# Performance work log

Measured on AMD Instinct MI355X. Metric: run time of the kernel, lower is better.

Reference implementation:

```python
import jax, jax.numpy as jnp
import numpy as np

B, T, I, H, O = 64, 512, 128, 1024, 128
FORGET_BIAS = 1.0  # TF LSTMCell default


def setup_inputs() -> dict:
    key = jax.random.key(0)
    k1, k2, k3 = jax.random.split(key, 3)
    X = jax.random.normal(k1, (B, T, I), dtype=jnp.float32)
    Wk = jax.random.normal(k2, (I + H, 4 * H), dtype=jnp.float32) * 0.02
    b = jnp.zeros((4 * H,), dtype=jnp.float32)
    Wd = jax.random.normal(k3, (H, O), dtype=jnp.float32) * 0.02
    bd = jnp.zeros((O,), dtype=jnp.float32)
    return {"X": X, "Wk": Wk, "b": b, "Wd": Wd, "bd": bd}


def _lstm(X, Wk, b):
    # TF LSTMCell with activation=relu; gate order in kernel: i, j, f, o
    batch = X.shape[0]
    h = X.shape[-1]  # not used; keep shapes explicit below
    c0 = jnp.zeros((batch, H), dtype=X.dtype)
    h0 = jnp.zeros((batch, H), dtype=X.dtype)

    def step(carry, x_t):
        c, hs = carry
        z = jnp.concatenate([x_t, hs], axis=-1) @ Wk + b  # [B, 4H]
        i, j, f, o = jnp.split(z, 4, axis=-1)
        i = jax.nn.sigmoid(i)
        f = jax.nn.sigmoid(f + FORGET_BIAS)
        o = jax.nn.sigmoid(o)
        g = jax.nn.relu(j)          # cell-input activation (custom relu)
        c_new = f * c + i * g
        h_new = o * jax.nn.relu(c_new)  # output activation (custom relu)
        return (c_new, h_new), h_new

    xs = jnp.swapaxes(X, 0, 1)  # [T, B, I]
    _, hs = jax.lax.scan(step, (c0, h0), xs)
    return jnp.swapaxes(hs, 0, 1)  # [B, T, H]


def reference(X, Wk, b, Wd, bd):
    rnn_out = _lstm(X, Wk, b)          # [B, T, H]
    outputs = rnn_out @ Wd + bd        # [B, T, O] (SL=True: dense per timestep)
    return outputs
```

## Files before the change

### kernel.cpp

```cpp
#include <hip/hip_runtime.h>
#include <math.h>

#define Bsz 64
#define Tn  512
#define In  128
#define Hn  1024
#define KT  1152
#define NBLK 128

#define GARR0 0
#define GFLG0 512

typedef __attribute__((ext_vector_type(8))) short bf16x8;
typedef __attribute__((ext_vector_type(4))) short s16x4;
typedef __attribute__((ext_vector_type(4))) float f32x4;
typedef __attribute__((ext_vector_type(4))) int   i32x4;

__device__ void llvm_amdgcn_raw_buffer_store_i16(short vdata, i32x4 srsrc, int voffset, int soffset, int cpol) __asm("llvm.amdgcn.raw.buffer.store.i16");

__device__ __forceinline__ i32x4 make_srd(const void* p, int bytes) {
  i32x4 r;
  r.x = (int)(unsigned)(unsigned long long)p;
  r.y = (int)((unsigned long long)p >> 32);
  r.z = bytes;
  r.w = 0x00020000;
  return r;
}

__device__ __forceinline__ unsigned short f2bf(float f) {
  union { float f; unsigned u; } x; x.f = f;
  unsigned r = x.u + 0x7FFFu + ((x.u >> 16) & 1u);
  return (unsigned short)(r >> 16);
}
__device__ __forceinline__ float sigmoidf_(float x) { return 1.0f / (1.0f + __expf(-x)); }

__global__ __launch_bounds__(256) void cast_x_kernel(const float* __restrict__ in,
                                                     unsigned short* __restrict__ out) {
  int i = blockIdx.x * 256 + threadIdx.x;
  f32x4 v = ((const f32x4*)in)[i];
  s16x4 o;
  o.x = (short)f2bf(v.x); o.y = (short)f2bf(v.y);
  o.z = (short)f2bf(v.z); o.w = (short)f2bf(v.w);
  ((s16x4*)out)[i] = o;
}

__global__ __launch_bounds__(256) void transpose_cast_kernel(const float* __restrict__ in,
                                                             unsigned short* __restrict__ out,
                                                             int R, int C, int ldo, int tilesR) {
  __shared__ unsigned short tile[64][73];
  int br = blockIdx.x % tilesR, bc = blockIdx.x / tilesR;
  int r0 = br << 6, c0 = bc << 6;
  for (int e = threadIdx.x; e < 4096; e += 256) {
    int r = e >> 6, c = e & 63;
    tile[r][c] = f2bf(in[(size_t)(r0 + r) * C + (c0 + c)]);
  }
  __syncthreads();
  for (int e = threadIdx.x; e < 4096; e += 256) {
    int c = e >> 6, r = e & 63;
    out[(size_t)(c0 + c) * ldo + (r0 + r)] = tile[r][c];
  }
}

__global__ __launch_bounds__(512, 1) void lstm_kernel(
    const unsigned short* __restrict__ Xb,
    const unsigned short* __restrict__ WkT,
    const float* __restrict__ bias,
    unsigned short* __restrict__ hs,
    unsigned* __restrict__ S)
{
  __shared__ float Z4[4][64][36];
  const int tid = threadIdx.x;
  const int blk = blockIdx.x;
  const int grp = blk >> 4;
  const int w   = tid >> 6;
  const int mh  = w & 1;
  const int kq  = w >> 1;
  const int l   = tid & 63, q = l >> 4, n16 = l & 15;

  const i32x4 hsrd = make_srd(hs, Tn * Bsz * Hn * 2);

  bf16x8 Bf[2][9];
#pragma unroll
  for (int nt = 0; nt < 2; ++nt) {
    int cl   = nt * 16 + n16;
    int gcol = (cl >> 3) * Hn + blk * 8 + (cl & 7);
    const unsigned short* bp = WkT + (size_t)gcol * KT + kq * 288 + q * 8;
#pragma unroll
    for (int ks = 0; ks < 9; ++ks)
      Bf[nt][ks] = *(const bf16x8*)(bp + ks * 32);
  }

  const int eb = tid >> 3, ej = tid & 7;
  const float bi  = bias[           blk * 8 + ej];
  const float bg  = bias[    Hn   + blk * 8 + ej];
  const float bfg = bias[2 * Hn   + blk * 8 + ej] + 1.0f;
  const float bo  = bias[3 * Hn   + blk * 8 + ej];
  const int   hst_off = (eb * Hn + blk * 8 + ej) * 2;
  float cst = 0.0f;

  const int b0 = mh * 32 + n16;
  const int b1 = b0 + 16;

  const unsigned needm = (kq == 0) ? 0x03u : (kq == 1) ? 0x0Eu : (kq == 2) ? 0x38u : 0xE0u;
  const bool mine = (l < 8) && ((needm >> l) & 1u);

  for (int t = 0; t < Tn; ++t) {
    f32x4 a00 = {0,0,0,0}, a01 = {0,0,0,0}, a10 = {0,0,0,0}, a11 = {0,0,0,0};

    if (t > 0) {
      bf16x8 X0[4], X1[4];
      if (kq == 0) {
#pragma unroll
        for (int ks = 0; ks < 4; ++ks) {
          X0[ks] = *(const bf16x8*)(Xb + ((size_t)b0 * Tn + t) * In + ks * 32 + q * 8);
          X1[ks] = *(const bf16x8*)(Xb + ((size_t)b1 * Tn + t) * In + ks * 32 + q * 8);
        }
      }
      for (;;) {
        unsigned f = mine ? __hip_atomic_load(&S[GFLG0 + 32 * l], __ATOMIC_RELAXED,
                                              __HIP_MEMORY_SCOPE_AGENT)
                          : 0xFFFFFFFFu;
        if (__ballot(f >= (unsigned)t) == ~0ull) break;
        __builtin_amdgcn_s_sleep(1);
      }
      const unsigned short* hrow = hs + (size_t)(t - 1) * (Bsz * Hn);
#pragma unroll
      for (int ks = 0; ks < 9; ++ks) {
        bf16x8 A0, A1;
        if (kq == 0 && ks < 4) {
          A0 = X0[ks]; A1 = X1[ks];
        } else {
          int kh = kq * 288 + ks * 32 - 128 + q * 8;
          A0 = *(const bf16x8*)(hrow + (size_t)b0 * Hn + kh);
          A1 = *(const bf16x8*)(hrow + (size_t)b1 * Hn + kh);
        }
        a00 = __builtin_amdgcn_mfma_f32_16x16x32_bf16(A0, Bf[0][ks], a00, 0, 0, 0);
        a01 = __builtin_amdgcn_mfma_f32_16x16x32_bf16(A0, Bf[1][ks], a01, 0, 0, 0);
        a10 = __builtin_amdgcn_mfma_f32_16x16x32_bf16(A1, Bf[0][ks], a10, 0, 0, 0);
        a11 = __builtin_amdgcn_mfma_f32_16x16x32_bf16(A1, Bf[1][ks], a11, 0, 0, 0);
      }
    } else if (kq == 0) {
#pragma unroll
      for (int ks = 0; ks < 4; ++ks) {
        bf16x8 A0 = *(const bf16x8*)(Xb + ((size_t)b0 * Tn) * In + ks * 32 + q * 8);
        bf16x8 A1 = *(const bf16x8*)(Xb + ((size_t)b1 * Tn) * In + ks * 32 + q * 8);
        a00 = __builtin_amdgcn_mfma_f32_16x16x32_bf16(A0, Bf[0][ks], a00, 0, 0, 0);
        a01 = __builtin_amdgcn_mfma_f32_16x16x32_bf16(A0, Bf[1][ks], a01, 0, 0, 0);
        a10 = __builtin_amdgcn_mfma_f32_16x16x32_bf16(A1, Bf[0][ks], a10, 0, 0, 0);
        a11 = __builtin_amdgcn_mfma_f32_16x16x32_bf16(A1, Bf[1][ks], a11, 0, 0, 0);
      }
    }

#pragma unroll
    for (int r = 0; r < 4; ++r) {
      int row = mh * 32 + q * 4 + r;
      Z4[kq][row     ][     n16] = a00[r];
      Z4[kq][row     ][16 + n16] = a01[r];
      Z4[kq][row + 16][     n16] = a10[r];
      Z4[kq][row + 16][16 + n16] = a11[r];
    }
    __syncthreads();

    float zi = bi, zg = bg, zf = bfg, zo = bo;
#pragma unroll
    for (int k2 = 0; k2 < 4; ++k2) {
      zi += Z4[k2][eb][     ej];
      zg += Z4[k2][eb][ 8 + ej];
      zf += Z4[k2][eb][16 + ej];
      zo += Z4[k2][eb][24 + ej];
    }
    float ig = sigmoidf_(zi);
    float g  = fmaxf(zg, 0.0f);
    float ff = sigmoidf_(zf);
    float oo = sigmoidf_(zo);
    cst = ff * cst + ig * g;
    float hn = oo * fmaxf(cst, 0.0f);
    llvm_amdgcn_raw_buffer_store_i16((short)f2bf(hn), hsrd,
                                     t * (Bsz * Hn * 2) + hst_off, 0, 17);

    __syncthreads();
    if (t < Tn - 1 && tid == 0) {
      const unsigned tgt = (unsigned)t + 1u;
      unsigned old = __hip_atomic_fetch_add(&S[GARR0 + 32 * grp], 1u,
                                            __ATOMIC_RELAXED, __HIP_MEMORY_SCOPE_AGENT);
      if (old == 16u * tgt - 1u)
        __hip_atomic_store(&S[GFLG0 + 32 * grp], tgt,
                           __ATOMIC_RELAXED, __HIP_MEMORY_SCOPE_AGENT);
    }
  }
}

__global__ __launch_bounds__(256) void dense_kernel(
    const unsigned short* __restrict__ hs,
    const unsigned short* __restrict__ WdT,
    const float* __restrict__ bd,
    float* __restrict__ out)
{
  const int tid = threadIdx.x;
  const int w = tid >> 6, l = tid & 63, q = l >> 4, n16 = l & 15;
  const int R0 = blockIdx.x * 64 + w * 16;
  f32x4 acc[8];
#pragma unroll
  for (int i = 0; i < 8; ++i) acc[i] = (f32x4){0, 0, 0, 0};
  const unsigned short* arow = hs + (size_t)(R0 + n16) * Hn + q * 8;
#pragma unroll 4
  for (int ks = 0; ks < 32; ++ks) {
    bf16x8 A = *(const bf16x8*)(arow + ks * 32);
#pragma unroll
    for (int nt = 0; nt < 8; ++nt) {
      bf16x8 Bf = *(const bf16x8*)(WdT + (size_t)(nt * 16 + n16) * Hn + ks * 32 + q * 8);
      acc[nt] = __builtin_amdgcn_mfma_f32_16x16x32_bf16(A, Bf, acc[nt], 0, 0, 0);
    }
  }
#pragma unroll
  for (int nt = 0; nt < 8; ++nt) {
    int col = nt * 16 + n16;
    float bdv = bd[col];
#pragma unroll
    for (int r = 0; r < 4; ++r) {
      int R = R0 + q * 4 + r;
      int b = R & 63, t = R >> 6;
      out[((size_t)b * Tn + t) * 128 + col] = acc[nt][r] + bdv;
    }
  }
}

extern "C" void kernel_launch(void* const* d_in, const int* in_sizes, int n_in,
                              void* d_out, int out_size, void* d_ws, size_t ws_size,
                              hipStream_t stream) {
  const float* X    = (const float*)d_in[0];
  const float* Wk   = (const float*)d_in[1];
  const float* bias = (const float*)d_in[2];
  const float* Wd   = (const float*)d_in[3];
  const float* bd   = (const float*)d_in[4];
  float* out = (float*)d_out;

  char* ws = (char*)d_ws;
  unsigned short* Xb  = (unsigned short*)(ws);
  unsigned short* WkT = (unsigned short*)(ws + 8388608);
  unsigned short* WdT = (unsigned short*)(ws + 17825792);
  unsigned short* hs  = (unsigned short*)(ws + 18087936);
  unsigned*       syn = (unsigned*)      (ws + 85196800);

  hipMemsetAsync(syn, 0, 4096, stream);
  cast_x_kernel<<<4096, 256, 0, stream>>>(X, Xb);
  transpose_cast_kernel<<<1152, 256, 0, stream>>>(Wk, WkT, 1152, 4096, 1152, 18);
  transpose_cast_kernel<<<32, 256, 0, stream>>>(Wd, WdT, 1024, 128, 1024, 16);
  lstm_kernel<<<NBLK, 512, 0, stream>>>(Xb, WkT, bias, hs, syn);
  dense_kernel<<<512, 256, 0, stream>>>(hs, WdT, bd, out);
}
```

Before: 3.026 ms.

## Replace group-counter barrier with per-block flags and vectorized staged h stores

```diff
diff --git a/kernel.cpp b/kernel.cpp
--- a/kernel.cpp
+++ b/kernel.cpp
@@ -8,15 +8,14 @@
 #define KT  1152
 #define NBLK 128
 
-#define GARR0 0
-#define GFLG0 512
-
 typedef __attribute__((ext_vector_type(8))) short bf16x8;
 typedef __attribute__((ext_vector_type(4))) short s16x4;
 typedef __attribute__((ext_vector_type(4))) float f32x4;
 typedef __attribute__((ext_vector_type(4))) int   i32x4;
 
-__device__ void llvm_amdgcn_raw_buffer_store_i16(short vdata, i32x4 srsrc, int voffset, int soffset, int cpol) __asm("llvm.amdgcn.raw.buffer.store.i16");
+__device__ void llvm_amdgcn_raw_buffer_store_i32x4(i32x4 vdata, i32x4 srsrc, int voffset, int soffset, int cpol) __asm("llvm.amdgcn.raw.buffer.store.v4i32");
+
+union B128 { i32x4 i; bf16x8 h; };
 
 __device__ __forceinline__ i32x4 make_srd(const void* p, int bytes) {
   i32x4 r;
@@ -25,6 +24,10 @@
   r.z = bytes;
   r.w = 0x00020000;
   return r;
+}
+
+__device__ __forceinline__ void bar_lds() {
+  asm volatile("s_waitcnt lgkmcnt(0)\n\ts_barrier" ::: "memory");
 }
 
 __device__ __forceinline__ unsigned short f2bf(float f) {
@@ -69,9 +72,9 @@
     unsigned* __restrict__ S)
 {
   __shared__ float Z4[4][64][36];
+  __shared__ unsigned short hstage[64][8];
   const int tid = threadIdx.x;
   const int blk = blockIdx.x;
-  const int grp = blk >> 4;
   const int w   = tid >> 6;
   const int mh  = w & 1;
   const int kq  = w >> 1;
@@ -95,14 +98,15 @@
   const float bg  = bias[    Hn   + blk * 8 + ej];
   const float bfg = bias[2 * Hn   + blk * 8 + ej] + 1.0f;
   const float bo  = bias[3 * Hn   + blk * 8 + ej];
-  const int   hst_off = (eb * Hn + blk * 8 + ej) * 2;
   float cst = 0.0f;
 
   const int b0 = mh * 32 + n16;
   const int b1 = b0 + 16;
 
-  const unsigned needm = (kq == 0) ? 0x03u : (kq == 1) ? 0x0Eu : (kq == 2) ? 0x38u : 0xE0u;
-  const bool mine = (l < 8) && ((needm >> l) & 1u);
+  const int pfirst = (kq == 0) ? 0 : (kq == 1) ? 20 : (kq == 2) ? 56 : 92;
+  const int pcnt   = (kq == 0) ? 20 : 36;
+  const bool mine  = (l < pcnt);
+  const int  pidx  = pfirst + (mine ? l : 0);
 
   for (int t = 0; t < Tn; ++t) {
     f32x4 a00 = {0,0,0,0}, a01 = {0,0,0,0}, a10 = {0,0,0,0}, a11 = {0,0,0,0};
@@ -117,7 +121,7 @@
         }
       }
       for (;;) {
-        unsigned f = mine ? __hip_atomic_load(&S[GFLG0 + 32 * l], __ATOMIC_RELAXED,
+        unsigned f = mine ? __hip_atomic_load(&S[pidx], __ATOMIC_RELAXED,
                                               __HIP_MEMORY_SCOPE_AGENT)
                           : 0xFFFFFFFFu;
         if (__ballot(f >= (unsigned)t) == ~0ull) break;
@@ -159,7 +163,7 @@
       Z4[kq][row + 16][     n16] = a10[r];
       Z4[kq][row + 16][16 + n16] = a11[r];
     }
-    __syncthreads();
+    bar_lds();
 
     float zi = bi, zg = bg, zf = bfg, zo = bo;
 #pragma unroll
@@ -175,17 +179,19 @@
     float oo = sigmoidf_(zo);
     cst = ff * cst + ig * g;
     float hn = oo * fmaxf(cst, 0.0f);
-    llvm_amdgcn_raw_buffer_store_i16((short)f2bf(hn), hsrd,
-                                     t * (Bsz * Hn * 2) + hst_off, 0, 17);
-
-    __syncthreads();
-    if (t < Tn - 1 && tid == 0) {
-      const unsigned tgt = (unsigned)t + 1u;
-      unsigned old = __hip_atomic_fetch_add(&S[GARR0 + 32 * grp], 1u,
-                                            __ATOMIC_RELAXED, __HIP_MEMORY_SCOPE_AGENT);
-      if (old == 16u * tgt - 1u)
-        __hip_atomic_store(&S[GFLG0 + 32 * grp], tgt,
-                           __ATOMIC_RELAXED, __HIP_MEMORY_SCOPE_AGENT);
+    hstage[eb][ej] = f2bf(hn);
+    bar_lds();
+
+    if (w == 0) {
+      B128 v; v.h = *(const bf16x8*)&hstage[l][0];
+      llvm_amdgcn_raw_buffer_store_i32x4(v.i, hsrd,
+          t * (Bsz * Hn * 2) + l * (Hn * 2) + blk * 16, 0, 17);
+      if (t < Tn - 1) {
+        asm volatile("s_waitcnt vmcnt(0)" ::: "memory");
+        if (tid == 0)
+          __hip_atomic_store(&S[blk], (unsigned)(t + 1),
+                             __ATOMIC_RELAXED, __HIP_MEMORY_SCOPE_AGENT);
+      }
     }
   }
 }
@@ -242,7 +248,7 @@
   unsigned short* hs  = (unsigned short*)(ws + 18087936);
   unsigned*       syn = (unsigned*)      (ws + 85196800);
 
-  hipMemsetAsync(syn, 0, 4096, stream);
+  hipMemsetAsync(syn, 0, 512, stream);
   cast_x_kernel<<<4096, 256, 0, stream>>>(X, Xb);
   transpose_cast_kernel<<<1152, 256, 0, stream>>>(Wk, WkT, 1152, 4096, 1152, 18);
   transpose_cast_kernel<<<32, 256, 0, stream>>>(Wd, WdT, 1024, 128, 1024, 16);
```

Result: slower. 3.914 ms (+29.4%).
